# Kernel tuning notes

Hardware: AMD Instinct MI355X
Metric: run time of the kernel (lower is better)

## Reference

```python
import jax, jax.numpy as jnp
import numpy as np

L = 19          # kernel size (hardcoded 19x19 views in the original)
HH = WW = 256   # hardcoded fold output_size=(256,256)


def _patches(x, l):
    # x: (Hp, Wp) -> (H, W, l, l) sliding windows (stride 1, valid)
    h = x.shape[0] - l + 1
    w = x.shape[1] - l + 1
    r = jnp.arange(h)[:, None] + jnp.arange(l)[None, :]   # (h, l)
    c = jnp.arange(w)[:, None] + jnp.arange(l)[None, :]   # (w, l)
    return x[r[:, None, :, None], c[None, :, None, :]]    # (h, w, l, l)


def setup_inputs() -> dict:
    key = jax.random.key(0)
    k1, k2 = jax.random.split(key)
    inp = jax.random.normal(k1, (1, 3, HH, WW), dtype=jnp.float32)
    ker = jax.random.uniform(k2, (L, L, HH, WW), dtype=jnp.float32)
    return {"input": inp, "kernel": ker}


def _forward(inp, ker):
    l = L
    B, C, h, w = inp.shape  # B must be 1 (original reshapes assume it)
    p2 = l // 2
    pad = jnp.pad(inp, ((0, 0), (0, 0), (p2, p2), (p2, p2)), mode="reflect")
    k = ker
    out_unf = None
    for i in range(3):  # replicates the original channel loop (only last kept)
        p = _patches(pad[0, i], l)                        # (h, w, l, l)
        # torch F.unfold layout: (l*l kernel-pos row-major, h*w spatial row-major)
        unf = p.transpose(2, 3, 0, 1).reshape(l * l, h * w)
        # torch: (1, l*l, h*w) -> reshape(1, h*w, 1, l, l); row-major reflatten
        dg = unf.reshape(h * w, l, l)
        # kernel: permute(2,3,0,1) + contiguous().view(-1,1,l,l), reassigned
        # each iteration exactly as in the original module
        k = jnp.transpose(k, (2, 3, 0, 1)).reshape(-1, 1, l, l)
        k = k / jnp.sum(k, axis=(1, 2, 3), keepdims=True)
        # grouped conv with one group per pixel on (l,l) patch == per-pixel dot
        out = jnp.einsum("pab,pab->p", dg, k[:, 0])       # (h*w,)
        out_unf = out.reshape(1, 1, h, w)                 # fold with k=1
    return out_unf


def reference(input, kernel):
    return _forward(input, kernel)
```

## Files before the change

### kernel.cpp

```cpp
#include <hip/hip_runtime.h>

#define NPIX 65536
#define KK   361
#define LSZ  19
#define HWD  256
#define QB   16
#define CT   4
#define GPART 1024
#define NSLOT 8
#define NS2  16
#define SPS2 23
#define DTC  82

__device__ __forceinline__ int refl(int v) {
    v -= 9;
    v = v < 0 ? -v : v;
    v = v > 255 ? 510 - v : v;
    return v;
}

__global__ __launch_bounds__(256) void k_s1a(const float4* __restrict__ ker4,
                                             float4* __restrict__ part4) {
    const int p4 = blockIdx.x * 256 + threadIdx.x;
    const int strip = blockIdx.y;
    const int s0 = strip * SPS2;
    const int n = (strip == NS2 - 1) ? (KK - s0) : SPS2;
    const float4* kp = ker4 + (size_t)s0 * (NPIX / 4) + p4;
    float4 acc = {0.f, 0.f, 0.f, 0.f};
#pragma unroll 8
    for (int s = 0; s < n; ++s) {
        float4 v = kp[(size_t)s * (NPIX / 4)];
        acc.x += v.x; acc.y += v.y; acc.z += v.z; acc.w += v.w;
    }
    part4[(size_t)strip * (NPIX / 4) + p4] = acc;
}

__global__ __launch_bounds__(256) void k_s1b(const float4* __restrict__ part4,
                                             float4* __restrict__ rcp4) {
    const int i = blockIdx.x * 256 + threadIdx.x;
    float4 a = {0.f, 0.f, 0.f, 0.f};
#pragma unroll
    for (int s = 0; s < NS2; ++s) {
        float4 v = part4[(size_t)s * (NPIX / 4) + i];
        a.x += v.x; a.y += v.y; a.z += v.z; a.w += v.w;
    }
    rcp4[i] = float4{1.0f / a.x, 1.0f / a.y, 1.0f / a.z, 1.0f / a.w};
}

__global__ __launch_bounds__(384) void k_part(const float* __restrict__ ker,
                                              const float* __restrict__ rcpS1,
                                              const float* __restrict__ in2,
                                              float2* __restrict__ partial) {
    __shared__ float tile[QB * KK];
    __shared__ float dt[LSZ * DTC];
    __shared__ float rcpS2s[QB];
    const int tid = threadIdx.x;
    const int q0  = blockIdx.x * (QB * CT);

    {
        const int y0 = q0 >> 8, x0 = q0 & 255;
        for (int i = tid; i < LSZ * DTC; i += 384) {
            int a = i / DTC, c = i - a * DTC;
            dt[i] = in2[refl(y0 + a) * HWD + refl(x0 + c)];
        }
    }

    const int t  = tid;
    const int j0 = t * NPIX + q0;
    const int r0 = j0 / KK;
    const int jm = j0 - r0 * KK;
    const int d0 = (jm == 0) ? (QB * CT) : (KK - jm);
    const int split = d0 < (QB * CT) ? d0 : (QB * CT);
    const int a = t / LSZ, b = t - LSZ * a;
    const int dbase = a * DTC + b;
    float ad = 0.f, as = 0.f, sd = 0.f, ss = 0.f;

    for (int k = 0; k < CT; ++k) {
        __syncthreads();
        const int basek = (q0 + k * QB) * KK;
        const float4* k4 = (const float4*)(ker + basek);
        for (int i = tid; i < (QB * KK) / 4; i += 384) {
            float4 v = k4[i];
            int m = basek + i * 4;
            const float4 s = *(const float4*)(rcpS1 + (m & (NPIX - 1)));
            v.x *= s.x; v.y *= s.y; v.z *= s.z; v.w *= s.w;
            *(float4*)(tile + i * 4) = v;
        }
        __syncthreads();
        {
            int wave = tid >> 6, lane = tid & 63;
            for (int qq = wave; qq < QB; qq += 6) {
                float acc = 0.f;
                for (int e = lane; e < KK; e += 64) acc += tile[qq * KK + e];
                for (int m = 1; m < 64; m <<= 1) acc += __shfl_xor(acc, m);
                if (lane == 0) rcpS2s[qq] = 1.0f / acc;
            }
        }
        __syncthreads();
        if (t < KK) {
#pragma unroll
            for (int o = 0; o < QB; ++o) {
                int off = k * QB + o;
                if (off == split) { sd = ad; ss = as; }
                float v = tile[o * KK + t] * rcpS2s[o];
                float d = dt[dbase + off];
                ad += d * v;
                as += v;
            }
        }
    }

    if (t < KK) {
        const int slot = blockIdx.x & (NSLOT - 1);
        if (split == QB * CT) {
            partial[(size_t)r0 * NSLOT + slot] = float2{ad, as};
        } else {
            partial[(size_t)r0 * NSLOT + slot] = float2{sd, ss};
            partial[(size_t)(r0 + 1) * NSLOT + slot] = float2{ad - sd, as - ss};
        }
    }
}

__global__ __launch_bounds__(256) void k_out2(const float2* __restrict__ partial,
                                              float* __restrict__ out) {
    const int r = blockIdx.x * 256 + threadIdx.x;
    const int j0 = r * KK;
    const int qs = j0 & (NPIX - 1);
    const int ql = (j0 + KK - 1) & (NPIX - 1);
    const int first = qs >> 6;
    const int last  = ql >> 6;
    const int cnt = ((last - first) & (GPART - 1)) + 1;
    const float2* p = partial + (size_t)r * NSLOT;
    float dot = 0.f, sum = 0.f;
    for (int i = 0; i < cnt; ++i) {
        float2 v = p[(first + i) & (NSLOT - 1)];
        dot += v.x; sum += v.y;
    }
    out[r] = dot / sum;
}

__global__ __launch_bounds__(256) void k_s1(const float* __restrict__ ker,
                                            float* __restrict__ rcpS1) {
    int p = blockIdx.x * blockDim.x + threadIdx.x;
    const float* kp = ker + p;
    float a = 0.f;
    for (int s = 0; s < KK; ++s) a += kp[(size_t)s * NPIX];
    rcpS1[p] = 1.0f / a;
}

__global__ __launch_bounds__(256) void k_s2_fallback(const float* __restrict__ ker,
                                                     const float* __restrict__ rcpS1,
                                                     float* __restrict__ rcpS2) {
    int lane = threadIdx.x & 63;
    int q = blockIdx.x * 4 + (threadIdx.x >> 6);
    int base = q * KK;
    float acc = 0.f;
    for (int t = lane; t < KK; t += 64)
        acc += ker[base + t] * rcpS1[(base + t) & (NPIX - 1)];
    for (int m = 1; m < 64; m <<= 1) acc += __shfl_xor(acc, m);
    if (lane == 0) rcpS2[q] = 1.0f / acc;
}

__global__ __launch_bounds__(256) void k_out_fallback(const float* __restrict__ ker,
                                                      const float* __restrict__ rcpS1,
                                                      const float* __restrict__ rcpS2,
                                                      const float* __restrict__ in2,
                                                      float* __restrict__ out) {
    int lane = threadIdx.x & 63;
    int r = blockIdx.x * 4 + (threadIdx.x >> 6);
    float vsum = 0.f, vdot = 0.f;
    for (int u = lane; u < KK; u += 64) {
        int jj = r * KK + u;
        int t  = jj >> 16;
        int q  = jj & (NPIX - 1);
        int m  = q * KK + t;
        float v = ker[m] * rcpS1[m & (NPIX - 1)] * rcpS2[q];
        int y = q >> 8, x = q & 255;
        int a = t / LSZ, b = t - a * LSZ;
        float d = in2[refl(y + a) * HWD + refl(x + b)];
        vsum += v;
        vdot += d * v;
    }
    for (int mm = 1; mm < 64; mm <<= 1) {
        vsum += __shfl_xor(vsum, mm);
        vdot += __shfl_xor(vdot, mm);
    }
    if (lane == 0) out[r] = vdot / vsum;
}

extern "C" void kernel_launch(void* const* d_in, const int* in_sizes, int n_in,
                              void* d_out, int out_size, void* d_ws, size_t ws_size,
                              hipStream_t stream) {
    const float* inp = (const float*)d_in[0];
    const float* ker = (const float*)d_in[1];
    float* out = (float*)d_out;
    const float* in2 = inp + 2 * NPIX;

    float*  rcpS1   = (float*)d_ws;
    float*  s1part  = rcpS1 + NPIX;
    float2* partial = (float2*)(s1part + (size_t)NS2 * NPIX);

    const size_t needed = ((size_t)NPIX * (1 + NS2) +
                           (size_t)NPIX * NSLOT * 2) * sizeof(float);

    if (ws_size >= needed) {
        dim3 g1(NPIX / 4 / 256, NS2);
        k_s1a<<<g1, 256, 0, stream>>>((const float4*)ker, (float4*)s1part);
        k_s1b<<<NPIX / 4 / 256, 256, 0, stream>>>((const float4*)s1part, (float4*)rcpS1);
        k_part<<<GPART, 384, 0, stream>>>(ker, rcpS1, in2, partial);
        k_out2<<<NPIX / 256, 256, 0, stream>>>(partial, out);
    } else {
        float* rcpS2 = rcpS1 + NPIX;
        k_s1<<<NPIX / 256, 256, 0, stream>>>(ker, rcpS1);
        k_s2_fallback<<<NPIX / 4, 256, 0, stream>>>(ker, rcpS1, rcpS2);
        k_out_fallback<<<NPIX / 4, 256, 0, stream>>>(ker, rcpS1, rcpS2, in2, out);
    }
}
```

Before: 51.42 us.

## Drop LDS kernel tile, read kernel directly from global and remap block order

```diff
diff --git a/kernel.cpp b/kernel.cpp
--- a/kernel.cpp
+++ b/kernel.cpp
@@ -4,9 +4,9 @@
 #define KK   361
 #define LSZ  19
 #define HWD  256
-#define QB   16
-#define CT   4
-#define GPART 1024
+#define CHUNK 64
+#define SUBT  16
+#define GPART (NPIX / CHUNK)
 #define NSLOT 8
 #define NS2  16
 #define SPS2 23
@@ -51,11 +51,11 @@
                                               const float* __restrict__ rcpS1,
                                               const float* __restrict__ in2,
                                               float2* __restrict__ partial) {
-    __shared__ float tile[QB * KK];
     __shared__ float dt[LSZ * DTC];
-    __shared__ float rcpS2s[QB];
+    __shared__ float rcpS2s[CHUNK];
     const int tid = threadIdx.x;
-    const int q0  = blockIdx.x * (QB * CT);
+    const int lb  = ((blockIdx.x & 7) << 7) | (blockIdx.x >> 3);
+    const int q0  = lb * CHUNK;
 
     {
         const int y0 = q0 >> 8, x0 = q0 & 255;
@@ -69,40 +69,32 @@
     const int j0 = t * NPIX + q0;
     const int r0 = j0 / KK;
     const int jm = j0 - r0 * KK;
-    const int d0 = (jm == 0) ? (QB * CT) : (KK - jm);
-    const int split = d0 < (QB * CT) ? d0 : (QB * CT);
+    const int d0 = (jm == 0) ? CHUNK : (KK - jm);
+    const int split = d0 < CHUNK ? d0 : CHUNK;
     const int a = t / LSZ, b = t - LSZ * a;
     const int dbase = a * DTC + b;
     float ad = 0.f, as = 0.f, sd = 0.f, ss = 0.f;
 
-    for (int k = 0; k < CT; ++k) {
-        __syncthreads();
-        const int basek = (q0 + k * QB) * KK;
-        const float4* k4 = (const float4*)(ker + basek);
-        for (int i = tid; i < (QB * KK) / 4; i += 384) {
-            float4 v = k4[i];
-            int m = basek + i * 4;
-            const float4 s = *(const float4*)(rcpS1 + (m & (NPIX - 1)));
-            v.x *= s.x; v.y *= s.y; v.z *= s.z; v.w *= s.w;
-            *(float4*)(tile + i * 4) = v;
-        }
-        __syncthreads();
-        {
-            int wave = tid >> 6, lane = tid & 63;
-            for (int qq = wave; qq < QB; qq += 6) {
-                float acc = 0.f;
-                for (int e = lane; e < KK; e += 64) acc += tile[qq * KK + e];
-                for (int m = 1; m < 64; m <<= 1) acc += __shfl_xor(acc, m);
-                if (lane == 0) rcpS2s[qq] = 1.0f / acc;
-            }
+    const int wave = tid >> 6, lane = tid & 63;
+
+    for (int k = 0; k < 4; ++k) {
+        for (int o = SUBT * k + wave; o < SUBT * (k + 1); o += 6) {
+            const int base = (q0 + o) * KK;
+            float acc = 0.f;
+#pragma unroll
+            for (int e = lane; e < KK; e += 64)
+                acc += ker[base + e] * rcpS1[(base + e) & (NPIX - 1)];
+            for (int m = 1; m < 64; m <<= 1) acc += __shfl_xor(acc, m);
+            if (lane == 0) rcpS2s[o] = 1.0f / acc;
         }
         __syncthreads();
         if (t < KK) {
 #pragma unroll
-            for (int o = 0; o < QB; ++o) {
-                int off = k * QB + o;
+            for (int oo = 0; oo < SUBT; ++oo) {
+                const int off = SUBT * k + oo;
                 if (off == split) { sd = ad; ss = as; }
-                float v = tile[o * KK + t] * rcpS2s[o];
+                const int m = (q0 + off) * KK + t;
+                float v = ker[m] * rcpS1[m & (NPIX - 1)] * rcpS2s[off];
                 float d = dt[dbase + off];
                 ad += d * v;
                 as += v;
@@ -111,8 +103,8 @@
     }
 
     if (t < KK) {
-        const int slot = blockIdx.x & (NSLOT - 1);
-        if (split == QB * CT) {
+        const int slot = lb & (NSLOT - 1);
+        if (split == CHUNK) {
             partial[(size_t)r0 * NSLOT + slot] = float2{ad, as};
         } else {
             partial[(size_t)r0 * NSLOT + slot] = float2{sd, ss};
```

Result: slower. 60.94 us (+18.5%).
